# Performance work log

Measured on AMD Instinct MI355X. Metric: run time of the kernel, lower is better.

Reference implementation:

```python
import jax, jax.numpy as jnp
import numpy as np

N, E, G, H, IN, OUT, L = 50000, 800000, 512, 128, 128, 10, 3
TH = 0.01  # filter_perm threshold


def setup_inputs() -> dict:
    key = jax.random.key(0)
    ks = jax.random.split(key, 16)
    s = 0.05
    return {
        "x": jax.random.normal(ks[0], (N, IN), jnp.float32),
        "edge_index": jax.random.randint(ks[1], (2, E), 0, N, jnp.int32),
        "batch": jnp.sort(jax.random.randint(ks[2], (N,), 0, G, jnp.int32)),
        "lin1_W": jax.random.normal(ks[3], (IN, H), jnp.float32) * s,
        "lin1_b": jnp.zeros((H,), jnp.float32),
        # per layer: [gcn_W, sage_Wn, sage_Ws, gin_W, gconv_Ws, gconv_Wn]
        "gnn_W": jax.random.normal(ks[4], (L, 6, H, H), jnp.float32) * s,
        "pool_p": jax.random.normal(ks[5], (L, 2, H), jnp.float32) * s,
        "lin_out_W": jax.random.normal(ks[6], (H, H), jnp.float32) * s,
        "lin_out_b": jnp.zeros((H,), jnp.float32),
        "cls_W": jax.random.normal(ks[7], (H, OUT), jnp.float32) * s,
        "cls_b": jnp.zeros((OUT,), jnp.float32),
        "na_log": 0.001 * jax.random.normal(ks[8], (L, 4), jnp.float32),
        "pool_log": 0.001 * jax.random.normal(ks[9], (L, 3), jnp.float32),
        "readout_log": 0.001 * jax.random.normal(ks[10], (L + 1, 3), jnp.float32),
        "la_log": 0.001 * jax.random.normal(ks[11], (1, 3), jnp.float32),
    }


def _readout(h, batch, w):
    # mixed readout: w0*mean + w1*max + w2*sum over graphs
    ssum = jax.ops.segment_sum(h, batch, num_segments=G)
    cnt = jax.ops.segment_sum(jnp.ones((h.shape[0], 1), h.dtype), batch, num_segments=G)
    mean = ssum / jnp.maximum(cnt, 1.0)
    smax = jax.ops.segment_max(h, batch, num_segments=G)
    smax = jnp.where(jnp.isfinite(smax), smax, 0.0)
    return w[0] * mean + w[1] * smax + w[2] * ssum


def reference(x, edge_index, batch, lin1_W, lin1_b, gnn_W, pool_p,
              lin_out_W, lin_out_b, cls_W, cls_b,
              na_log, pool_log, readout_log, la_log):
    na_a = jax.nn.softmax(na_log, -1)
    pool_a = jax.nn.softmax(pool_log, -1)
    ro_a = jax.nn.softmax(readout_log, -1)
    la_a = jax.nn.softmax(la_log, -1)

    # add self loops
    ar = jnp.arange(N, dtype=edge_index.dtype)
    src = jnp.concatenate([edge_index[0], ar])
    dst = jnp.concatenate([edge_index[1], ar])
    ew = jnp.ones(src.shape[0], jnp.float32)

    h = jax.nn.elu(x @ lin1_W + lin1_b)
    reps = [_readout(h, batch, ro_a[0])]

    for i in range(L):
        W = gnn_W[i]
        deg = jnp.maximum(jax.ops.segment_sum(ew, dst, num_segments=N), 1e-6)
        s_agg = jax.ops.segment_sum(h[src] * ew[:, None], dst, num_segments=N)  # [N,H]
        # gcn: symmetric-normalized aggregation of transformed features
        hg = h @ W[0]
        norm = ew * jax.lax.rsqrt(deg)[src] * jax.lax.rsqrt(deg)[dst]
        gcn = jax.ops.segment_sum(hg[src] * norm[:, None], dst, num_segments=N)
        sage = (s_agg / deg[:, None]) @ W[1] + h @ W[2]
        gin = (h + s_agg) @ W[3]
        gconv = h @ W[4] + s_agg @ W[5]
        a = na_a[i]
        h = a[0] * gcn + a[1] * sage + a[2] * gin + a[3] * gconv
        h = jax.nn.elu(h)
        # LayerNorm over the FULL tensor (normalized_shape = x.size()), no affine
        m = h.mean()
        v = jnp.mean((h - m) ** 2)
        h = (h - m) * jax.lax.rsqrt(v + 1e-5)
        # dropout identity (eval mode)
        # mixed pooling: score-gated soft pooling + filter_perm threshold mask
        g1 = jax.nn.sigmoid(h @ pool_p[i, 0])
        g2 = jnp.tanh(h @ pool_p[i, 1])
        pa = pool_a[i]
        gate = pa[0] * g1 + pa[1] * g2 + pa[2]  # third op = 'none' (gate 1)
        keep = (gate > TH).astype(h.dtype)
        h = h * (gate * keep)[:, None]
        ew = ew * keep[src] * keep[dst]
        reps.append(_readout(h, batch, ro_a[i + 1]))

    R = jnp.stack(reps)  # [L+1, G, H]
    la = la_a[0]
    z = la[0] * jax.nn.elu(R.sum(0)) + la[1] * jax.nn.elu(R.mean(0)) + la[2] * jax.nn.elu(R.max(0))
    z = jax.nn.elu(z @ lin_out_W + lin_out_b)
    logits = z @ cls_W + cls_b
    return jax.nn.log_softmax(logits, -1)
```

## Files before the change

### kernel.cpp

```cpp
#include <hip/hip_runtime.h>
#include <math.h>

#define NN 50000
#define EE 800000
#define GG 512
#define HH 128
#define LL 3
#define OUTC 10
#define THR 0.01f

typedef unsigned short u16;
typedef unsigned int u32;
typedef __attribute__((ext_vector_type(8))) short short8;
typedef __attribute__((ext_vector_type(4))) float f32x4;

__device__ __forceinline__ float elu_f(float x){ return x > 0.f ? x : (expf(x)-1.f); }
__device__ __forceinline__ u16 f2bf(float f){
    u32 u = __float_as_uint(f);
    return (u16)((u + 0x7fffu + ((u>>16)&1u)) >> 16);
}
__device__ __forceinline__ float bf2f(u16 b){ return __uint_as_float(((u32)b)<<16); }
__device__ __forceinline__ u32 pack2(float a, float b){
    return (u32)f2bf(a) | ((u32)f2bf(b)<<16);
}


__device__ void softmax_row(const float* in, float* out, int c){
    float m = in[0];
    for (int j=1;j<c;++j) m = fmaxf(m, in[j]);
    float s = 0.f;
    for (int j=0;j<c;++j){ float e = expf(in[j]-m); out[j]=e; s+=e; }
    for (int j=0;j<c;++j) out[j] /= s;
}

__global__ void prep_coef_k(const float* __restrict__ na, const float* __restrict__ pl,
                            const float* __restrict__ ro, const float* __restrict__ la,
                            float* __restrict__ coef){
    if (threadIdx.x != 0 || blockIdx.x != 0) return;
    for (int i=0;i<LL;++i)   softmax_row(na + i*4, coef + i*4, 4);
    for (int i=0;i<LL;++i)   softmax_row(pl + i*3, coef + 12 + i*3, 3);
    for (int i=0;i<LL+1;++i) softmax_row(ro + i*3, coef + 21 + i*3, 3);
    softmax_row(la, coef + 33, 3);
}

__global__ __launch_bounds__(256) void prep_w_k(const float* __restrict__ gW,
                                                const float* __restrict__ lin1W,
                                                const float* __restrict__ coef,
                                                u16* __restrict__ Wc, u16* __restrict__ lin1t){
    int idx = blockIdx.x*256 + threadIdx.x;
    const int total = LL*4*16384;
    if (idx < total){
        int i = idx >> 16;
        int rem = idx & 65535;
        int p = rem >> 14;
        int j = rem & 16383;
        int n = j >> 7, k = j & 127;
        const float* W = gW + (size_t)i*6*16384;
        float a0=coef[i*4], a1=coef[i*4+1], a2=coef[i*4+2], a3=coef[i*4+3];
        int e = k*128 + n;
        float v;
        if (p==0)      v = a1*W[2*16384+e] + a2*W[3*16384+e] + a3*W[4*16384+e];
        else if (p==1) v = a2*W[3*16384+e] + a3*W[5*16384+e];
        else if (p==2) v = a1*W[1*16384+e];
        else           v = a0*W[0*16384+e];
        Wc[(size_t)(i*4+p)*16384 + n*128 + k] = f2bf(v);
    } else if (idx < total + 16384){
        int j = idx - total;
        int n = j >> 7, k = j & 127;
        lin1t[n*128 + k] = f2bf(lin1W[k*128 + n]);
    }
}

__global__ void x2bf_k(const float* __restrict__ x, u16* __restrict__ xb){
    int i = blockIdx.x*256 + threadIdx.x;
    if (i >= NN*HH/8) return;
    const float4* p = (const float4*)x + (size_t)i*2;
    float4 v0 = p[0], v1 = p[1];
    uint4 o;
    o.x = pack2(v0.x, v0.y); o.y = pack2(v0.z, v0.w);
    o.z = pack2(v1.x, v1.y); o.w = pack2(v1.z, v1.w);
    ((uint4*)xb)[i] = o;
}

__global__ void count_k(const int* __restrict__ dst, int* __restrict__ counts){
    int e = blockIdx.x*256 + threadIdx.x;
    if (e < EE) atomicAdd(&counts[dst[e]], 1);
}

__global__ __launch_bounds__(256) void scan1_k(const int* __restrict__ counts,
                                               int* __restrict__ pre, int* __restrict__ bsum){
    int b = blockIdx.x, t = threadIdx.x;
    int base = b*1024 + t*4;
    int4 v = make_int4(0,0,0,0);
    if (base + 3 < NN) v = *(const int4*)(counts + base);
    else {
        int* pv = (int*)&v;
        #pragma unroll
        for (int j=0;j<4;++j) pv[j] = (base+j < NN) ? counts[base+j] : 0;
    }
    int s0 = v.x, s1 = s0+v.y, s2 = s1+v.z, s3 = s2+v.w;
    int lane = t & 63, w = t >> 6;
    int incl = s3;
    #pragma unroll
    for (int o=1;o<64;o<<=1){
        int u = __shfl_up(incl, o, 64);
        if (lane >= o) incl += u;
    }
    __shared__ int wsum[4];
    if (lane == 63) wsum[w] = incl;
    __syncthreads();
    int woff = 0;
    #pragma unroll
    for (int i=0;i<4;++i) if (i < w) woff += wsum[i];
    int excl = woff + incl - s3;
    int4 o4 = make_int4(excl, excl+s0, excl+s1, excl+s2);
    if (base + 3 < NN) *(int4*)(pre + base) = o4;
    else {
        int* po = (int*)&o4;
        for (int j=0;j<4;++j) if (base+j < NN) pre[base+j] = po[j];
    }
    if (t == 255) bsum[b] = woff + incl;
}

__global__ __launch_bounds__(256) void scan3_k(const int* __restrict__ pre,
                                               const int* __restrict__ bsum,
                                               int* __restrict__ row_ptr, int* __restrict__ cursor){
    int b = blockIdx.x, t = threadIdx.x;
    __shared__ int boff_s;
    if (t < 64){
        int v = (t < b) ? bsum[t] : 0;
        #pragma unroll
        for (int o=32;o>0;o>>=1) v += __shfl_down(v, o, 64);
        if (t == 0) boff_s = v;
    }
    __syncthreads();
    int boff = boff_s;
    int base = b*1024;
    #pragma unroll
    for (int j=0;j<4;++j){
        int i = base + j*256 + t;
        if (i < NN){
            int r = pre[i] + boff;
            row_ptr[i] = r;
            cursor[i] = r;
        }
    }
    if (b == 0 && t == 0) row_ptr[NN] = EE;
}

__global__ void initf_k(float* __restrict__ a, float v, int n){
    int i = blockIdx.x*256 + threadIdx.x;
    if (i < n) a[i] = v;
}

__global__ void fill_k(const int* __restrict__ src, const int* __restrict__ dst,
                       int* __restrict__ cursor, int* __restrict__ csr_src){
    int e = blockIdx.x*256 + threadIdx.x;
    if (e < EE){
        int p = atomicAdd(&cursor[dst[e]], 1);
        csr_src[p] = src[e];
    }
}

__global__ void gstart_k(const int* __restrict__ batch, int* __restrict__ gstart){
    int g = blockIdx.x*256 + threadIdx.x;
    if (g > GG) return;
    if (g == GG){ gstart[GG] = NN; return; }
    int lo = 0, hi = NN;
    while (lo < hi){
        int mid = (lo + hi) >> 1;
        if (batch[mid] < g) lo = mid + 1; else hi = mid;
    }
    gstart[g] = lo;
}

template<int FLAGS, int NP>
__global__ __launch_bounds__(256) void mm_k(
    const u16* __restrict__ A0, const u16* __restrict__ A1,
    const u16* __restrict__ A2, const u16* __restrict__ A3,
    const u16* __restrict__ Bb, const float* __restrict__ rowscale,
    const float* __restrict__ bias,
    u16* __restrict__ Cbf, double* __restrict__ stats, int M)
{
    int tid = threadIdx.x;
    int w = tid >> 6, l = tid & 63;
    int row0 = blockIdx.x * 128;
    int rbase = row0 + w*32 + (l & 15);
    int kq = l >> 4;
    const short8 zz = {0,0,0,0,0,0,0,0};

    f32x4 acc[2][8];
    #pragma unroll
    for (int rt=0;rt<2;++rt)
        #pragma unroll
        for (int ct=0;ct<8;++ct) acc[rt][ct] = (f32x4){0.f,0.f,0.f,0.f};

    auto do_pair = [&](const u16* __restrict__ Ap, const u16* __restrict__ Bp){
        #pragma unroll
        for (int ks=0; ks<4; ++ks){
            int ko = (ks*4 + kq)*8;
            short8 a[2], b[8];
            #pragma unroll
            for (int rt=0; rt<2; ++rt){
                int gr = rbase + rt*16;
                a[rt] = (gr < M) ? *(const short8*)(Ap + (size_t)gr*128 + ko) : zz;
            }
            #pragma unroll
            for (int ct=0; ct<8; ++ct)
                b[ct] = *(const short8*)(Bp + (ct*16 + (l&15))*128 + ko);
            #pragma unroll
            for (int rt=0; rt<2; ++rt)
                #pragma unroll
                for (int ct=0; ct<8; ++ct)
                    acc[rt][ct] = __builtin_amdgcn_mfma_f32_16x16x32_bf16(a[rt], b[ct], acc[rt][ct], 0, 0, 0);
        }
    };

    if constexpr (NP == 4){
        do_pair(A2, Bb + 2*16384);
        #pragma unroll
        for (int rt=0; rt<2; ++rt){
            #pragma unroll
            for (int i=0; i<4; ++i){
                int row = row0 + w*32 + rt*16 + (l>>4)*4 + i;
                float d = (row < M) ? rowscale[row] : 0.f;
                #pragma unroll
                for (int ct=0; ct<8; ++ct) acc[rt][ct][i] *= d;
            }
        }
        do_pair(A0, Bb);
        do_pair(A1, Bb + 16384);
        do_pair(A3, Bb + 3*16384);
    } else {
        do_pair(A0, Bb);
    }

    float ls = 0.f, lq = 0.f;
    float bcol[8];
    if constexpr (FLAGS & 2){
        #pragma unroll
        for (int ct=0; ct<8; ++ct) bcol[ct] = bias[ct*16 + (l&15)];
    }
    #pragma unroll
    for (int rt=0; rt<2; ++rt){
        #pragma unroll
        for (int i=0; i<4; ++i){
            int row = row0 + w*32 + rt*16 + (l>>4)*4 + i;
            if (row >= M) continue;
            #pragma unroll
            for (int ct=0; ct<8; ++ct){
                float v = acc[rt][ct][i];
                if constexpr (FLAGS & 2) v += bcol[ct];
                v = elu_f(v);
                Cbf[(size_t)row*128 + ct*16 + (l&15)] = f2bf(v);
                if constexpr (FLAGS & 1){ ls += v; lq = fmaf(v, v, lq); }
            }
        }
    }
    if constexpr (FLAGS & 1){
        double s = ls, q = lq;
        #pragma unroll
        for (int o=32;o>0;o>>=1){ s += __shfl_xor(s,o,64); q += __shfl_xor(q,o,64); }
        __shared__ double sw[4], qw[4];
        if (l == 0){ sw[w] = s; qw[w] = q; }
        __syncthreads();
        if (tid == 0){
            atomicAdd(&stats[0], sw[0]+sw[1]+sw[2]+sw[3]);
            atomicAdd(&stats[1], qw[0]+qw[1]+qw[2]+qw[3]);
        }
    }
}


__global__ __launch_bounds__(256) void deg2_k(const int* __restrict__ rp, const int* __restrict__ cs,
                                              const float* __restrict__ alive,
                                              float2* __restrict__ ar2, float* __restrict__ invdeg){
    int n = (blockIdx.x*256 + threadIdx.x) >> 6;
    int lane = threadIdx.x & 63;
    if (n >= NN) return;
    int e0 = rp[n], e1 = rp[n+1];
    float c = 0.f;
    for (int e = e0 + lane; e < e1; e += 64) c += alive[cs[e]];
    #pragma unroll
    for (int o=32;o>0;o>>=1) c += __shfl_xor(c, o, 64);
    if (lane == 0){
        float al = alive[n];
        float d = (al == 0.f) ? 1e-6f : fmaxf(1.f + c, 1e-6f);
        ar2[n] = make_float2(al, al * rsqrtf(d));
        invdeg[n] = 1.f / d;
    }
}

__global__ __launch_bounds__(256) void agg_k(const u16* __restrict__ h,
    const int* __restrict__ rp, const int* __restrict__ cs,
    const float2* __restrict__ ar2,
    u16* __restrict__ sagg, u16* __restrict__ gagg){
    int n = (blockIdx.x*256 + threadIdx.x) >> 6;
    int lane = threadIdx.x & 63;
    if (n >= NN) return;
    float2 an = ar2[n];
    u32* so = (u32*)(sagg + (size_t)n*HH);
    u32* go = (u32*)(gagg + (size_t)n*HH);
    if (an.x == 0.f){ so[lane]=0u; go[lane]=0u; return; }
    float rn = an.y;
    int e0 = rp[n], e1 = rp[n+1];
    float sx=0.f, sy=0.f, gx=0.f, gy=0.f;
    for (int e = e0; e < e1; e += 4){
        int lastv = e1 - 1;
        int x1 = e+1 <= lastv ? e+1 : lastv;
        int x2 = e+2 <= lastv ? e+2 : lastv;
        int x3 = e+3 <= lastv ? e+3 : lastv;
        int s0 = cs[e], s1 = cs[x1], s2 = cs[x2], s3 = cs[x3];
        float2 w0 = ar2[s0], w1 = ar2[s1], w2 = ar2[s2], w3 = ar2[s3];
        if (e+1 > lastv){ w1.x = 0.f; w1.y = 0.f; }
        if (e+2 > lastv){ w2.x = 0.f; w2.y = 0.f; }
        if (e+3 > lastv){ w3.x = 0.f; w3.y = 0.f; }
        u32 h0 = *(const u32*)(h + (size_t)s0*HH + lane*2);
        u32 h1 = *(const u32*)(h + (size_t)s1*HH + lane*2);
        u32 h2 = *(const u32*)(h + (size_t)s2*HH + lane*2);
        u32 h3 = *(const u32*)(h + (size_t)s3*HH + lane*2);
        float ax, ay;
        ax = bf2f((u16)(h0 & 0xffffu)); ay = bf2f((u16)(h0 >> 16));
        sx = fmaf(w0.x, ax, sx); sy = fmaf(w0.x, ay, sy);
        gx = fmaf(w0.y, ax, gx); gy = fmaf(w0.y, ay, gy);
        ax = bf2f((u16)(h1 & 0xffffu)); ay = bf2f((u16)(h1 >> 16));
        sx = fmaf(w1.x, ax, sx); sy = fmaf(w1.x, ay, sy);
        gx = fmaf(w1.y, ax, gx); gy = fmaf(w1.y, ay, gy);
        ax = bf2f((u16)(h2 & 0xffffu)); ay = bf2f((u16)(h2 >> 16));
        sx = fmaf(w2.x, ax, sx); sy = fmaf(w2.x, ay, sy);
        gx = fmaf(w2.y, ax, gx); gy = fmaf(w2.y, ay, gy);
        ax = bf2f((u16)(h3 & 0xffffu)); ay = bf2f((u16)(h3 >> 16));
        sx = fmaf(w3.x, ax, sx); sy = fmaf(w3.x, ay, sy);
        gx = fmaf(w3.y, ax, gx); gy = fmaf(w3.y, ay, gy);
    }
    u32 hn = *(const u32*)(h + (size_t)n*HH + lane*2);
    float hx = bf2f((u16)(hn & 0xffffu)), hy = bf2f((u16)(hn >> 16));
    sx += hx; sy += hy;
    gx = fmaf(rn, hx, gx); gy = fmaf(rn, hy, gy);
    so[lane] = pack2(sx, sy);
    go[lane] = pack2(rn*gx, rn*gy);
}

__global__ __launch_bounds__(1024) void lnro_k(u16* __restrict__ hb,
                                               const double* __restrict__ stats,
                                               const float* __restrict__ p0,
                                               const float* __restrict__ p1,
                                               const float* __restrict__ pa,
                                               const float* __restrict__ row,
                                               const int* __restrict__ gstart,
                                               float* __restrict__ alive,
                                               float* __restrict__ rep){
    int g = blockIdx.x, tid = threadIdx.x;
    int w = tid >> 6, lane = tid & 63;
    int beg = gstart[g], end = gstart[g+1];
    const double tot = (double)NN * (double)HH;
    double m = stats[0] / tot;
    double var = stats[1] / tot - m*m;
    float mf = (float)m;
    float rs = rsqrtf((float)var + 1e-5f);
    float2 q0 = ((const float2*)p0)[lane];
    float2 q1 = ((const float2*)p1)[lane];
    float pa0 = pa[0], pa1 = pa[1], pa2 = pa[2];
    float csx = 0.f, csy = 0.f, cmx = -INFINITY, cmy = -INFINITY;
    for (int n = beg + w; n < end; n += 16){
        u32 hv = ((u32*)(hb + (size_t)n*HH))[lane];
        float vx = (bf2f((u16)(hv & 0xffffu)) - mf) * rs;
        float vy = (bf2f((u16)(hv >> 16))    - mf) * rs;
        float d0 = vx*q0.x + vy*q0.y;
        float d1 = vx*q1.x + vy*q1.y;
        #pragma unroll
        for (int o=32;o>0;o>>=1){ d0 += __shfl_xor(d0,o,64); d1 += __shfl_xor(d1,o,64); }
        float g1 = 1.f/(1.f + expf(-d0));
        float g2 = tanhf(d1);
        float gate = pa0*g1 + pa1*g2 + pa2;
        float keep = gate > THR ? 1.f : 0.f;
        float sc = gate*keep;
        vx *= sc; vy *= sc;
        ((u32*)(hb + (size_t)n*HH))[lane] = pack2(vx, vy);
        if (lane == 0 && keep == 0.f) alive[n] = 0.f;
        csx += vx; csy += vy;
        cmx = fmaxf(cmx, vx); cmy = fmaxf(cmy, vy);
    }
    __shared__ float ls[16][HH];
    __shared__ float lm[16][HH];
    ls[w][2*lane] = csx; ls[w][2*lane+1] = csy;
    lm[w][2*lane] = cmx; lm[w][2*lane+1] = cmy;
    __syncthreads();
    if (tid < HH){
        float s = 0.f, mx = -INFINITY;
        #pragma unroll
        for (int i=0;i<16;++i){ s += ls[i][tid]; mx = fmaxf(mx, lm[i][tid]); }
        if (mx == -INFINITY) mx = 0.f;
        float cnt = (float)(end - beg);
        float mean = s / fmaxf(cnt, 1.f);
        rep[(size_t)g*HH + tid] = row[0]*mean + row[1]*mx + row[2]*s;
    }
}

__global__ __launch_bounds__(1024) void readout_k(const u16* __restrict__ h,
                                                  const int* __restrict__ gstart,
                                                  const float* __restrict__ w,
                                                  float* __restrict__ rep){
    int g = blockIdx.x;
    int t = threadIdx.x & 127, q = threadIdx.x >> 7;
    int beg = gstart[g], end = gstart[g+1];
    float sum = 0.f, mx = -INFINITY;
    for (int n = beg + q; n < end; n += 8){
        float v = bf2f(h[(size_t)n*HH + t]);
        sum += v;
        mx = fmaxf(mx, v);
    }
    __shared__ float ss[8][HH];
    __shared__ float ms[8][HH];
    ss[q][t] = sum; ms[q][t] = mx;
    __syncthreads();
    if (threadIdx.x < HH){
        float s = 0.f, m = -INFINITY;
        #pragma unroll
        for (int i=0;i<8;++i){ s += ss[i][threadIdx.x]; m = fmaxf(m, ms[i][threadIdx.x]); }
        if (m == -INFINITY) m = 0.f;
        float cnt = (float)(end - beg);
        float mean = s / fmaxf(cnt, 1.f);
        rep[(size_t)g*HH + threadIdx.x] = w[0]*mean + w[1]*m + w[2]*s;
    }
}

__global__ __launch_bounds__(128) void final_k(const float* __restrict__ reps,
                                               const float* __restrict__ la,
                                               const float* __restrict__ loW,
                                               const float* __restrict__ lob,
                                               const float* __restrict__ cW,
                                               const float* __restrict__ cb,
                                               float* __restrict__ out){
    int g = blockIdx.x, t = threadIdx.x;
    float r0 = reps[(size_t)(0*GG+g)*HH + t];
    float r1 = reps[(size_t)(1*GG+g)*HH + t];
    float r2 = reps[(size_t)(2*GG+g)*HH + t];
    float r3 = reps[(size_t)(3*GG+g)*HH + t];
    float s = r0+r1+r2+r3;
    float mean = 0.25f*s;
    float mx = fmaxf(fmaxf(r0,r1), fmaxf(r2,r3));
    float z = la[0]*elu_f(s) + la[1]*elu_f(mean) + la[2]*elu_f(mx);
    __shared__ float zs[HH];
    zs[t] = z;
    __syncthreads();
    float a = lob[t];
    for (int k=0;k<HH;++k) a = fmaf(zs[k], loW[(size_t)k*HH + t], a);
    float z2 = elu_f(a);
    __shared__ float z2s[HH];
    z2s[t] = z2;
    __syncthreads();
    __shared__ float lg[OUTC];
    if (t < OUTC){
        float acc = cb[t];
        for (int k=0;k<HH;++k) acc = fmaf(z2s[k], cW[(size_t)k*OUTC + t], acc);
        lg[t] = acc;
    }
    __syncthreads();
    if (t == 0){
        float m = lg[0];
        for (int o=1;o<OUTC;++o) m = fmaxf(m, lg[o]);
        float se = 0.f;
        for (int o=0;o<OUTC;++o) se += expf(lg[o]-m);
        float lse = m + logf(se);
        for (int o=0;o<OUTC;++o) out[(size_t)g*OUTC + o] = lg[o] - lse;
    }
}


extern "C" void kernel_launch(void* const* d_in, const int* in_sizes, int n_in,
                              void* d_out, int out_size, void* d_ws, size_t ws_size,
                              hipStream_t stream){
    const float* x     = (const float*)d_in[0];
    const int*   ei    = (const int*)d_in[1];
    const int*   batch = (const int*)d_in[2];
    const float* l1W   = (const float*)d_in[3];
    const float* l1b   = (const float*)d_in[4];
    const float* gW    = (const float*)d_in[5];
    const float* poolp = (const float*)d_in[6];
    const float* loW   = (const float*)d_in[7];
    const float* lob   = (const float*)d_in[8];
    const float* cW    = (const float*)d_in[9];
    const float* cb    = (const float*)d_in[10];
    const float* nalog = (const float*)d_in[11];
    const float* pllog = (const float*)d_in[12];
    const float* rolog = (const float*)d_in[13];
    const float* lalog = (const float*)d_in[14];
    float* out = (float*)d_out;

    char* wsb = (char*)d_ws;
    size_t off = 0;
    auto alloc = [&](size_t bytes)->char* {
        char* p = wsb + off;
        off += (bytes + 255) & ~(size_t)255;
        return p;
    };
    u16*   hb     = (u16*)alloc(sizeof(u16)*(size_t)NN*HH);
    u16*   xb     = (u16*)alloc(sizeof(u16)*(size_t)NN*HH);
    u16*   sagg   = (u16*)alloc(sizeof(u16)*(size_t)NN*HH);
    u16*   gagg   = (u16*)alloc(sizeof(u16)*(size_t)NN*HH);
    u16*   Wc     = (u16*)alloc(sizeof(u16)*(size_t)LL*4*HH*HH);
    u16*   lin1t  = (u16*)alloc(sizeof(u16)*HH*HH);
    int*   row_ptr= (int*)alloc(sizeof(int)*(NN+1));
    int*   counts = (int*)alloc(sizeof(int)*NN);
    int*   cursor = (int*)alloc(sizeof(int)*NN);
    int*   pre    = (int*)alloc(sizeof(int)*NN);
    int*   bsum   = (int*)alloc(sizeof(int)*64);
    int*   csr_src= (int*)alloc(sizeof(int)*EE);
    float2* ar2   = (float2*)alloc(sizeof(float2)*NN);
    float* invdeg = (float*)alloc(sizeof(float)*NN);
    float* alive  = (float*)alloc(sizeof(float)*NN);
    int*   gstart = (int*)alloc(sizeof(int)*(GG+1));
    float* reps   = (float*)alloc(sizeof(float)*(size_t)(LL+1)*GG*HH);
    float* coef   = (float*)alloc(sizeof(float)*64);
    double* stats = (double*)alloc(sizeof(double)*2*LL);

    const int* srcp = ei;
    const int* dstp = ei + EE;

    hipMemsetAsync(counts, 0, sizeof(int)*NN, stream);
    hipMemsetAsync(stats, 0, sizeof(double)*2*LL, stream);

    const int SCAN_BLOCKS = (NN + 1023)/1024;

    prep_coef_k<<<1, 64, 0, stream>>>(nalog, pllog, rolog, lalog, coef);
    prep_w_k<<<(LL*4*16384 + 16384 + 255)/256, 256, 0, stream>>>(gW, l1W, coef, Wc, lin1t);
    count_k<<<(EE + 255)/256, 256, 0, stream>>>(dstp, counts);
    scan1_k<<<SCAN_BLOCKS, 256, 0, stream>>>(counts, pre, bsum);
    scan3_k<<<SCAN_BLOCKS, 256, 0, stream>>>(pre, bsum, row_ptr, cursor);
    fill_k<<<(EE + 255)/256, 256, 0, stream>>>(srcp, dstp, cursor, csr_src);
    gstart_k<<<(GG + 256)/256, 256, 0, stream>>>(batch, gstart);
    initf_k<<<(NN + 255)/256, 256, 0, stream>>>(alive, 1.f, NN);
    x2bf_k<<<(NN*HH/8 + 255)/256, 256, 0, stream>>>(x, xb);

    const int gemm_blocks = (NN + 127)/128;

    mm_k<2,1><<<gemm_blocks, 256, 0, stream>>>(xb, nullptr, nullptr, nullptr,
                                               lin1t, nullptr, l1b, hb, nullptr, NN);
    readout_k<<<GG, 1024, 0, stream>>>(hb, gstart, coef + 21, reps);

    for (int i=0;i<LL;++i){
        deg2_k<<<(NN + 3)/4, 256, 0, stream>>>(row_ptr, csr_src, alive, ar2, invdeg);
        agg_k<<<(NN + 3)/4, 256, 0, stream>>>(hb, row_ptr, csr_src, ar2, sagg, gagg);
        mm_k<1,4><<<gemm_blocks, 256, 0, stream>>>(hb, sagg, sagg, gagg,
                                                   Wc + (size_t)i*4*16384, invdeg, nullptr,
                                                   hb, stats + 2*i, NN);
        lnro_k<<<GG, 1024, 0, stream>>>(hb, stats + 2*i,
                                        poolp + (size_t)(i*2+0)*HH,
                                        poolp + (size_t)(i*2+1)*HH,
                                        coef + 12 + i*3,
                                        coef + 21 + (i+1)*3,
                                        gstart, alive,
                                        reps + (size_t)(i+1)*GG*HH);
    }

    final_k<<<GG, HH, 0, stream>>>(reps, coef + 33, loW, lob, cW, cb, out);
}
```

Measured before the change: 606.1 us.

## Pad CSR rows to multiples of four with sentinel node to drop tail masking

Each node's CSR row is rounded up to a multiple of four and padded with a sentinel index NN, whose alive flag and ar2 weights are zero. The aggregation loop can then load four neighbours per step without clamping or masking. agg_k is also relaunched as one 64-thread block per node. The cost is a larger edge array, an extra padding kernel, and some wasted gathers of the sentinel row. deg2_k now also reads the padded edges, but these contribute zero because alive[NN]=0.

```diff
diff --git a/kernel.cpp b/kernel.cpp
--- a/kernel.cpp
+++ b/kernel.cpp
@@ -98,6 +98,7 @@
         #pragma unroll
         for (int j=0;j<4;++j) pv[j] = (base+j < NN) ? counts[base+j] : 0;
     }
+    v.x = (v.x+3)&~3; v.y = (v.y+3)&~3; v.z = (v.z+3)&~3; v.w = (v.w+3)&~3;
     int s0 = v.x, s1 = s0+v.y, s2 = s1+v.z, s3 = s2+v.w;
     int lane = t & 63, w = t >> 6;
     int incl = s3;
@@ -145,12 +146,12 @@
             cursor[i] = r;
         }
     }
-    if (b == 0 && t == 0) row_ptr[NN] = EE;
-}
-
-__global__ void initf_k(float* __restrict__ a, float v, int n){
+    if (b == (int)gridDim.x - 1 && t == 0) row_ptr[NN] = boff + bsum[b];
+}
+
+__global__ void init_alive_k(float* __restrict__ a){
     int i = blockIdx.x*256 + threadIdx.x;
-    if (i < n) a[i] = v;
+    if (i <= NN) a[i] = (i < NN) ? 1.f : 0.f;
 }
 
 __global__ void fill_k(const int* __restrict__ src, const int* __restrict__ dst,
@@ -160,6 +161,14 @@
         int p = atomicAdd(&cursor[dst[e]], 1);
         csr_src[p] = src[e];
     }
+}
+
+__global__ void pad_fill_k(const int* __restrict__ cursor, const int* __restrict__ row_ptr,
+                           int* __restrict__ csr_src){
+    int n = blockIdx.x*256 + threadIdx.x;
+    if (n >= NN) return;
+    int e1 = row_ptr[n+1];
+    for (int p = cursor[n]; p < e1; ++p) csr_src[p] = NN;
 }
 
 __global__ void gstart_k(const int* __restrict__ batch, int* __restrict__ gstart){
@@ -275,6 +284,7 @@
 __global__ __launch_bounds__(256) void deg2_k(const int* __restrict__ rp, const int* __restrict__ cs,
                                               const float* __restrict__ alive,
                                               float2* __restrict__ ar2, float* __restrict__ invdeg){
+    if (blockIdx.x == 0 && threadIdx.x == 0) ar2[NN] = make_float2(0.f, 0.f);
     int n = (blockIdx.x*256 + threadIdx.x) >> 6;
     int lane = threadIdx.x & 63;
     if (n >= NN) return;
@@ -291,13 +301,12 @@
     }
 }
 
-__global__ __launch_bounds__(256) void agg_k(const u16* __restrict__ h,
+__global__ __launch_bounds__(64) void agg_k(const u16* __restrict__ h,
     const int* __restrict__ rp, const int* __restrict__ cs,
     const float2* __restrict__ ar2,
     u16* __restrict__ sagg, u16* __restrict__ gagg){
-    int n = (blockIdx.x*256 + threadIdx.x) >> 6;
-    int lane = threadIdx.x & 63;
-    if (n >= NN) return;
+    int n = blockIdx.x;
+    int lane = threadIdx.x;
     float2 an = ar2[n];
     u32* so = (u32*)(sagg + (size_t)n*HH);
     u32* go = (u32*)(gagg + (size_t)n*HH);
@@ -306,19 +315,12 @@
     int e0 = rp[n], e1 = rp[n+1];
     float sx=0.f, sy=0.f, gx=0.f, gy=0.f;
     for (int e = e0; e < e1; e += 4){
-        int lastv = e1 - 1;
-        int x1 = e+1 <= lastv ? e+1 : lastv;
-        int x2 = e+2 <= lastv ? e+2 : lastv;
-        int x3 = e+3 <= lastv ? e+3 : lastv;
-        int s0 = cs[e], s1 = cs[x1], s2 = cs[x2], s3 = cs[x3];
-        float2 w0 = ar2[s0], w1 = ar2[s1], w2 = ar2[s2], w3 = ar2[s3];
-        if (e+1 > lastv){ w1.x = 0.f; w1.y = 0.f; }
-        if (e+2 > lastv){ w2.x = 0.f; w2.y = 0.f; }
-        if (e+3 > lastv){ w3.x = 0.f; w3.y = 0.f; }
-        u32 h0 = *(const u32*)(h + (size_t)s0*HH + lane*2);
-        u32 h1 = *(const u32*)(h + (size_t)s1*HH + lane*2);
-        u32 h2 = *(const u32*)(h + (size_t)s2*HH + lane*2);
-        u32 h3 = *(const u32*)(h + (size_t)s3*HH + lane*2);
+        int i0 = cs[e], i1 = cs[e+1], i2 = cs[e+2], i3 = cs[e+3];
+        float2 w0 = ar2[i0], w1 = ar2[i1], w2 = ar2[i2], w3 = ar2[i3];
+        u32 h0 = *(const u32*)(h + (size_t)i0*HH + lane*2);
+        u32 h1 = *(const u32*)(h + (size_t)i1*HH + lane*2);
+        u32 h2 = *(const u32*)(h + (size_t)i2*HH + lane*2);
+        u32 h3 = *(const u32*)(h + (size_t)i3*HH + lane*2);
         float ax, ay;
         ax = bf2f((u16)(h0 & 0xffffu)); ay = bf2f((u16)(h0 >> 16));
         sx = fmaf(w0.x, ax, sx); sy = fmaf(w0.x, ay, sy);
@@ -495,7 +497,8 @@
         off += (bytes + 255) & ~(size_t)255;
         return p;
     };
-    u16*   hb     = (u16*)alloc(sizeof(u16)*(size_t)NN*HH);
+    const int EEP = EE + 3*NN + 16;
+    u16*   hb     = (u16*)alloc(sizeof(u16)*(size_t)(NN+1)*HH);
     u16*   xb     = (u16*)alloc(sizeof(u16)*(size_t)NN*HH);
     u16*   sagg   = (u16*)alloc(sizeof(u16)*(size_t)NN*HH);
     u16*   gagg   = (u16*)alloc(sizeof(u16)*(size_t)NN*HH);
@@ -506,10 +509,10 @@
     int*   cursor = (int*)alloc(sizeof(int)*NN);
     int*   pre    = (int*)alloc(sizeof(int)*NN);
     int*   bsum   = (int*)alloc(sizeof(int)*64);
-    int*   csr_src= (int*)alloc(sizeof(int)*EE);
-    float2* ar2   = (float2*)alloc(sizeof(float2)*NN);
+    int*   csr_src= (int*)alloc(sizeof(int)*EEP);
+    float2* ar2   = (float2*)alloc(sizeof(float2)*(NN+1));
     float* invdeg = (float*)alloc(sizeof(float)*NN);
-    float* alive  = (float*)alloc(sizeof(float)*NN);
+    float* alive  = (float*)alloc(sizeof(float)*(NN+1));
     int*   gstart = (int*)alloc(sizeof(int)*(GG+1));
     float* reps   = (float*)alloc(sizeof(float)*(size_t)(LL+1)*GG*HH);
     float* coef   = (float*)alloc(sizeof(float)*64);
@@ -529,8 +532,9 @@
     scan1_k<<<SCAN_BLOCKS, 256, 0, stream>>>(counts, pre, bsum);
     scan3_k<<<SCAN_BLOCKS, 256, 0, stream>>>(pre, bsum, row_ptr, cursor);
     fill_k<<<(EE + 255)/256, 256, 0, stream>>>(srcp, dstp, cursor, csr_src);
+    pad_fill_k<<<(NN + 255)/256, 256, 0, stream>>>(cursor, row_ptr, csr_src);
     gstart_k<<<(GG + 256)/256, 256, 0, stream>>>(batch, gstart);
-    initf_k<<<(NN + 255)/256, 256, 0, stream>>>(alive, 1.f, NN);
+    init_alive_k<<<(NN + 256)/256, 256, 0, stream>>>(alive);
     x2bf_k<<<(NN*HH/8 + 255)/256, 256, 0, stream>>>(x, xb);
 
     const int gemm_blocks = (NN + 127)/128;
@@ -541,7 +545,7 @@
 
     for (int i=0;i<LL;++i){
         deg2_k<<<(NN + 3)/4, 256, 0, stream>>>(row_ptr, csr_src, alive, ar2, invdeg);
-        agg_k<<<(NN + 3)/4, 256, 0, stream>>>(hb, row_ptr, csr_src, ar2, sagg, gagg);
+        agg_k<<<NN, 64, 0, stream>>>(hb, row_ptr, csr_src, ar2, sagg, gagg);
         mm_k<1,4><<<gemm_blocks, 256, 0, stream>>>(hb, sagg, sagg, gagg,
                                                    Wc + (size_t)i*4*16384, invdeg, nullptr,
                                                    hb, stats + 2*i, NN);
```

Result: faster. 566.1 us (-6.6%).
